# Kernel optimization log

Hardware: AMD Instinct MI355X
Metric: run time of the kernel (lower is better)

Reference implementation:

```python
import jax, jax.numpy as jnp
import numpy as np

N_NODES = 50000
N_EDGES = 800000
IN_F = 128
HID = 64
OUT_F = 64
H = 1  # num_heads


def _gat_layer(x, W, al, ar, b, src, dst, n_nodes):
    # DGL GATConv: project, per-head attention logits, edge softmax over dst, scatter-sum
    h, f = al.shape
    feat = (x @ W).reshape(x.shape[0], h, f)              # [N,H,F]
    el = jnp.sum(feat * al, axis=-1)                       # [N,H]
    er = jnp.sum(feat * ar, axis=-1)                       # [N,H]
    e = jax.nn.leaky_relu(el[src] + er[dst], negative_slope=0.2)  # [E,H]
    emax = jax.ops.segment_max(e, dst, num_segments=n_nodes)      # [N,H]
    ex = jnp.exp(e - emax[dst])                            # [E,H]
    denom = jax.ops.segment_sum(ex, dst, num_segments=n_nodes)    # [N,H]
    alpha = ex / denom[dst]                                # [E,H] edge softmax
    msg = feat[src] * alpha[:, :, None]                    # [E,H,F]
    out = jax.ops.segment_sum(msg, dst, num_segments=n_nodes) + b # [N,H,F]
    return out


def setup_inputs() -> dict:
    key = jax.random.key(0)
    ks = jax.random.split(key, 20)

    def glorot(k, shape, fan_in):
        return jax.random.normal(k, shape, dtype=jnp.float32) / np.sqrt(fan_in)

    x = jax.random.normal(ks[0], (N_NODES, IN_F), dtype=jnp.float32)
    src = jax.random.randint(ks[1], (N_EDGES,), 0, N_NODES, dtype=jnp.int32)
    dst = jax.random.randint(ks[2], (N_EDGES,), 0, N_NODES, dtype=jnp.int32)
    neg_src = jax.random.randint(ks[3], (N_EDGES,), 0, N_NODES, dtype=jnp.int32)
    neg_dst = jax.random.randint(ks[4], (N_EDGES,), 0, N_NODES, dtype=jnp.int32)

    # layer dims: 128 -> 64 -> 128 -> 64 (hidden, hidden*2, out), H=1, mean over heads
    W1 = glorot(ks[5], (IN_F, H * HID), IN_F)
    al1 = glorot(ks[6], (H, HID), HID)
    ar1 = glorot(ks[7], (H, HID), HID)
    b1 = jnp.zeros((H, HID), dtype=jnp.float32)
    W2 = glorot(ks[8], (HID, H * 2 * HID), HID)
    al2 = glorot(ks[9], (H, 2 * HID), 2 * HID)
    ar2 = glorot(ks[10], (H, 2 * HID), 2 * HID)
    b2 = jnp.zeros((H, 2 * HID), dtype=jnp.float32)
    W3 = glorot(ks[11], (2 * HID, H * OUT_F), 2 * HID)
    al3 = glorot(ks[12], (H, OUT_F), OUT_F)
    ar3 = glorot(ks[13], (H, OUT_F), OUT_F)
    b3 = jnp.zeros((H, OUT_F), dtype=jnp.float32)
    lp_W = glorot(ks[14], (2 * OUT_F, 1), 2 * OUT_F)
    lp_b = jnp.zeros((1,), dtype=jnp.float32)

    return {
        "x": x, "W1": W1, "al1": al1, "ar1": ar1, "b1": b1,
        "W2": W2, "al2": al2, "ar2": ar2, "b2": b2,
        "W3": W3, "al3": al3, "ar3": ar3, "b3": b3,
        "lp_W": lp_W, "lp_b": lp_b,
        "src": src, "dst": dst, "neg_src": neg_src, "neg_dst": neg_dst,
    }


def reference(x, W1, al1, ar1, b1, W2, al2, ar2, b2, W3, al3, ar3, b3,
              lp_W, lp_b, src, dst, neg_src, neg_dst):
    n = x.shape[0]
    h = jax.nn.relu(_gat_layer(x, W1, al1, ar1, b1, src, dst, n)).mean(axis=1)
    h = jax.nn.relu(_gat_layer(h, W2, al2, ar2, b2, src, dst, n)).mean(axis=1)
    h = _gat_layer(h, W3, al3, ar3, b3, src, dst, n).mean(axis=1)      # [N,OUT_F]
    pos_score = (jnp.concatenate([h[src], h[dst]], axis=1) @ lp_W + lp_b)[:, 0]
    neg_score = (jnp.concatenate([h[neg_src], h[neg_dst]], axis=1) @ lp_W + lp_b)[:, 0]
    return h, pos_score, neg_score
```

## Files before the change

### kernel.cpp

```cpp
#include <hip/hip_runtime.h>
#include <hip/hip_bf16.h>

#define NN 50000
#define NE 800000
#define NBKT 196
#define NT 200
#define TILE 4000

typedef unsigned short ushort_t;
typedef unsigned int uint_t;

typedef __bf16 bf16_t;
typedef bf16_t bf16x8 __attribute__((ext_vector_type(8)));
typedef float f32x4 __attribute__((ext_vector_type(4)));

__device__ __forceinline__ float leaky(float v) { return (v >= 0.f) ? v : 0.2f * v; }
__device__ __forceinline__ ushort_t f2bf(float f) {
    __hip_bfloat16 h = __float2bfloat16(f);
    return *reinterpret_cast<ushort_t*>(&h);
}
__device__ __forceinline__ float bf_lo(uint_t v) { return __uint_as_float(v << 16); }
__device__ __forceinline__ float bf_hi(uint_t v) { return __uint_as_float(v & 0xFFFF0000u); }


#define XBLK 3125
#define WELEM (128 * 64 * 3)
#define WBLK 96

__global__ void prep_hist(const float* __restrict__ X, ushort_t* __restrict__ Xbf,
                          const float* __restrict__ W1, const float* __restrict__ W2,
                          const float* __restrict__ W3, ushort_t* __restrict__ Wt1,
                          ushort_t* __restrict__ Wt2, ushort_t* __restrict__ Wt3,
                          const float* __restrict__ al2, const float* __restrict__ ar2,
                          float* __restrict__ val2, float* __restrict__ var2,
                          const int* __restrict__ dst, uint_t* __restrict__ gh) {
    __shared__ uint_t h[NBKT];
    int tid = threadIdx.x;
    int blk = blockIdx.x;
    if (blk < NT) {
        for (int i = tid; i < NBKT; i += 256) h[i] = 0;
        __syncthreads();
        int e0 = blk * TILE;
        for (int i = tid; i < TILE; i += 256)
            atomicAdd(&h[((uint_t)dst[e0 + i]) >> 8], 1u);
        __syncthreads();
        for (int i = tid; i < NBKT; i += 256) gh[(size_t)i * NT + blk] = h[i];
        return;
    }
    blk -= NT;
    if (blk < XBLK) {
        int i = blk * 256 + tid;
        const float4* p = reinterpret_cast<const float4*>(X + (size_t)i * 8);
        float4 a = p[0], b = p[1];
        uint4 o;
        o.x = ((uint_t)f2bf(a.y) << 16) | f2bf(a.x);
        o.y = ((uint_t)f2bf(a.w) << 16) | f2bf(a.z);
        o.z = ((uint_t)f2bf(b.y) << 16) | f2bf(b.x);
        o.w = ((uint_t)f2bf(b.w) << 16) | f2bf(b.z);
        *reinterpret_cast<uint4*>(Xbf + (size_t)i * 8) = o;
        return;
    }
    blk -= XBLK;
    if (blk < WBLK) {
        int gw = blk * 256 + tid;
        if (gw < 128 * 64) {
            int i = gw; int k = i >> 6, m = i & 63;
            Wt1[m * 128 + k] = f2bf(W1[i]);
        } else if (gw < 2 * 128 * 64) {
            int i = gw - 128 * 64; int k = i >> 7, m = i & 127;
            Wt2[m * 64 + k] = f2bf(W2[i]);
        } else if (gw < WELEM) {
            int i = gw - 2 * 128 * 64; int k = i >> 6, m = i & 63;
            Wt3[m * 128 + k] = f2bf(W3[i]);
        }
        return;
    }
    if (tid < 128) {
        int k = tid & 63;
        const float* av = (tid < 64) ? al2 : ar2;
        float acc = 0.f;
        const float* row = W2 + k * 128;
        #pragma unroll 8
        for (int m = 0; m < 128; ++m) acc += row[m] * av[m];
        if (tid < 64) val2[k] = acc; else var2[k] = acc;
    }
}


__global__ void scan_gh(uint_t* __restrict__ gh, uint_t* __restrict__ bucketbase) {
    int b = threadIdx.x;
    uint_t run = 0;
    if (b < NBKT) {
        uint_t* row = gh + (size_t)b * NT;
        #pragma unroll 8
        for (int t = 0; t < NT; ++t) { uint_t v = row[t]; row[t] = run; run += v; }
    }
    int lane = b & 63, w = b >> 6;
    uint_t sc = run;
    for (int o = 1; o < 64; o <<= 1) {
        uint_t x = __shfl_up(sc, o);
        if (lane >= o) sc += x;
    }
    __shared__ uint_t ws4[4];
    if (lane == 63) ws4[w] = sc;
    __syncthreads();
    if (b == 0) { uint_t r = 0; for (int i = 0; i < 4; ++i) { uint_t tmp = ws4[i]; ws4[i] = r; r += tmp; } }
    __syncthreads();
    uint_t excl = ws4[w] + sc - run;
    if (b < NBKT) {
        bucketbase[b] = excl;
        uint_t* row = gh + (size_t)b * NT;
        #pragma unroll 8
        for (int t = 0; t < NT; ++t) row[t] += excl;
    }
    if (b == NBKT - 1) bucketbase[NBKT] = excl + run;
}

__global__ void part_scatter(const int* __restrict__ src, const int* __restrict__ dst,
                             const uint_t* __restrict__ gh, uint_t* __restrict__ pairbuf) {
    __shared__ uint_t cur[NBKT];
    int t = blockIdx.x, tid = threadIdx.x;
    for (int i = tid; i < NBKT; i += 256) cur[i] = gh[(size_t)i * NT + t];
    __syncthreads();
    int e0 = t * TILE;
    for (int i = tid; i < TILE; i += 256) {
        int d = dst[e0 + i], s = src[e0 + i];
        uint_t pos = atomicAdd(&cur[((uint_t)d) >> 8], 1u);
        pairbuf[pos] = (uint_t)s | (((uint_t)d & 255u) << 16);
    }
}

__device__ __forceinline__ void gemm64_core(const ushort_t* __restrict__ Xbf,
                                            const ushort_t* __restrict__ Wt,
                                            const float* __restrict__ al,
                                            const float* __restrict__ ar,
                                            ushort_t* __restrict__ featbf,
                                            float* __restrict__ el, float* __restrict__ er,
                                            int N, int blk, int tid) {
    constexpr int CT = 4, KI = 4;
    int wv = tid >> 6, lane = tid & 63;
    int c = lane & 15, kq = lane >> 4;
    int n0 = blk * 64 + wv * 16;
    if (n0 >= N) return;

    const ushort_t* aptr = Xbf + (size_t)(n0 + c) * 128 + kq * 8;
    bf16x8 a[KI];
    #pragma unroll
    for (int ki = 0; ki < KI; ++ki)
        a[ki] = *reinterpret_cast<const bf16x8*>(aptr + ki * 32);

    f32x4 acc[CT];
    #pragma unroll
    for (int ct = 0; ct < CT; ++ct) acc[ct] = (f32x4){0.f, 0.f, 0.f, 0.f};

    #pragma unroll
    for (int ct = 0; ct < CT; ++ct) {
        const ushort_t* bptr = Wt + (size_t)(ct * 16 + c) * 128 + kq * 8;
        #pragma unroll
        for (int ki = 0; ki < KI; ++ki) {
            bf16x8 b = *reinterpret_cast<const bf16x8*>(bptr + ki * 32);
            acc[ct] = __builtin_amdgcn_mfma_f32_16x16x32_bf16(a[ki], b, acc[ct], 0, 0, 0);
        }
    }

    float pe[4] = {0.f, 0.f, 0.f, 0.f}, pr[4] = {0.f, 0.f, 0.f, 0.f};
    #pragma unroll
    for (int ct = 0; ct < CT; ++ct) {
        float alv = al[ct * 16 + c], arv = ar[ct * 16 + c];
        #pragma unroll
        for (int j = 0; j < 4; ++j) {
            float v = acc[ct][j];
            featbf[(size_t)(n0 + kq * 4 + j) * 64 + ct * 16 + c] = f2bf(v);
            pe[j] += v * alv;
            pr[j] += v * arv;
        }
    }
    #pragma unroll
    for (int o = 1; o < 16; o <<= 1) {
        #pragma unroll
        for (int j = 0; j < 4; ++j) {
            pe[j] += __shfl_xor(pe[j], o);
            pr[j] += __shfl_xor(pr[j], o);
        }
    }
    if (c == 0) {
        #pragma unroll
        for (int j = 0; j < 4; ++j) {
            el[n0 + kq * 4 + j] = pe[j];
            er[n0 + kq * 4 + j] = pr[j];
        }
    }
}

__global__ void csr_gemm1(const uint_t* __restrict__ pairbuf, const uint_t* __restrict__ bucketbase,
                          int* __restrict__ off, int* __restrict__ csrsrc,
                          const ushort_t* __restrict__ Xbf, const ushort_t* __restrict__ Wt1,
                          const float* __restrict__ al1, const float* __restrict__ ar1,
                          ushort_t* __restrict__ featbf, float* __restrict__ el,
                          float* __restrict__ er, int N) {
    __shared__ uint_t cnt[256];
    __shared__ uint_t ws4[4];
    int tid = threadIdx.x;
    if (blockIdx.x >= NBKT) {
        gemm64_core(Xbf, Wt1, al1, ar1, featbf, el, er, N, blockIdx.x - NBKT, tid);
        return;
    }
    int b = blockIdx.x;
    uint_t eb0 = bucketbase[b], m = bucketbase[b + 1] - eb0;
    cnt[tid] = 0;
    __syncthreads();
    for (uint_t i = tid; i < m; i += 256)
        atomicAdd(&cnt[pairbuf[eb0 + i] >> 16], 1u);
    __syncthreads();
    uint_t v = cnt[tid];
    int lane = tid & 63, w = tid >> 6;
    uint_t sc = v;
    for (int o = 1; o < 64; o <<= 1) {
        uint_t x = __shfl_up(sc, o);
        if (lane >= o) sc += x;
    }
    if (lane == 63) ws4[w] = sc;
    __syncthreads();
    if (tid == 0) { uint_t r = 0; for (int i = 0; i < 4; ++i) { uint_t tmp = ws4[i]; ws4[i] = r; r += tmp; } }
    __syncthreads();
    uint_t excl = ws4[w] + sc - v;
    int node = b * 256 + tid;
    if (node < NN) off[node] = (int)(eb0 + excl);
    if (b == 0 && tid == 0) off[NN] = NE;
    __syncthreads();
    cnt[tid] = eb0 + excl;
    __syncthreads();
    for (uint_t i = tid; i < m; i += 256) {
        uint_t p = pairbuf[eb0 + i];
        uint_t pos = atomicAdd(&cnt[p >> 16], 1u);
        csrsrc[pos] = (int)(p & 0xFFFFu);
    }
}

__global__ void fused_l23(const ushort_t* __restrict__ G, const ushort_t* __restrict__ Wt2,
                          const float* __restrict__ b2, const ushort_t* __restrict__ Wt3,
                          const float* __restrict__ al3, const float* __restrict__ ar3,
                          ushort_t* __restrict__ feat3, float* __restrict__ el,
                          float* __restrict__ er, int N) {
    __shared__ ushort_t h3s[4][16 * 128];
    int wv = threadIdx.x >> 6, lane = threadIdx.x & 63;
    int c = lane & 15, kq = lane >> 4;
    int n0 = blockIdx.x * 64 + wv * 16;
    if (n0 >= N) return;

    const ushort_t* aptr = G + (size_t)(n0 + c) * 64 + kq * 8;
    bf16x8 a1[2];
    a1[0] = *reinterpret_cast<const bf16x8*>(aptr);
    a1[1] = *reinterpret_cast<const bf16x8*>(aptr + 32);

    f32x4 acc2[8];
    #pragma unroll
    for (int ct = 0; ct < 8; ++ct) acc2[ct] = (f32x4){0.f, 0.f, 0.f, 0.f};
    #pragma unroll
    for (int ct = 0; ct < 8; ++ct) {
        const ushort_t* bptr = Wt2 + (size_t)(ct * 16 + c) * 64 + kq * 8;
        acc2[ct] = __builtin_amdgcn_mfma_f32_16x16x32_bf16(
            a1[0], *reinterpret_cast<const bf16x8*>(bptr), acc2[ct], 0, 0, 0);
        acc2[ct] = __builtin_amdgcn_mfma_f32_16x16x32_bf16(
            a1[1], *reinterpret_cast<const bf16x8*>(bptr + 32), acc2[ct], 0, 0, 0);
    }

    #pragma unroll
    for (int ct = 0; ct < 8; ++ct) {
        float bv = b2[ct * 16 + c];
        #pragma unroll
        for (int j = 0; j < 4; ++j) {
            int r = kq * 4 + j;
            float v = fmaxf(acc2[ct][j] + bv, 0.f);
            h3s[wv][r * 128 + ((ct * 16 + c) ^ ((r & 7) << 3))] = f2bf(v);
        }
    }

    bf16x8 a2[4];
    #pragma unroll
    for (int ki = 0; ki < 4; ++ki)
        a2[ki] = *reinterpret_cast<const bf16x8*>(
            &h3s[wv][c * 128 + ((ki * 32 + kq * 8) ^ ((c & 7) << 3))]);

    f32x4 acc3[4];
    #pragma unroll
    for (int ct = 0; ct < 4; ++ct) acc3[ct] = (f32x4){0.f, 0.f, 0.f, 0.f};
    #pragma unroll
    for (int ct = 0; ct < 4; ++ct) {
        const ushort_t* bptr = Wt3 + (size_t)(ct * 16 + c) * 128 + kq * 8;
        #pragma unroll
        for (int ki = 0; ki < 4; ++ki) {
            bf16x8 b = *reinterpret_cast<const bf16x8*>(bptr + ki * 32);
            acc3[ct] = __builtin_amdgcn_mfma_f32_16x16x32_bf16(a2[ki], b, acc3[ct], 0, 0, 0);
        }
    }

    float pe[4] = {0.f, 0.f, 0.f, 0.f}, pr[4] = {0.f, 0.f, 0.f, 0.f};
    #pragma unroll
    for (int ct = 0; ct < 4; ++ct) {
        float alv = al3[ct * 16 + c], arv = ar3[ct * 16 + c];
        #pragma unroll
        for (int j = 0; j < 4; ++j) {
            float v = acc3[ct][j];
            feat3[(size_t)(n0 + kq * 4 + j) * 64 + ct * 16 + c] = f2bf(v);
            pe[j] += v * alv;
            pr[j] += v * arv;
        }
    }
    #pragma unroll
    for (int o = 1; o < 16; o <<= 1) {
        #pragma unroll
        for (int j = 0; j < 4; ++j) {
            pe[j] += __shfl_xor(pe[j], o);
            pr[j] += __shfl_xor(pr[j], o);
        }
    }
    if (c == 0) {
        #pragma unroll
        for (int j = 0; j < 4; ++j) {
            el[n0 + kq * 4 + j] = pe[j];
            er[n0 + kq * 4 + j] = pr[j];
        }
    }
}

template <bool BIAS, bool RELU, bool BFOUT, bool DOTS>
__global__ void gat_agg2(const int* __restrict__ off, const int* __restrict__ csrsrc,
                         const float* __restrict__ el, const float* __restrict__ er,
                         const ushort_t* __restrict__ featbf, const float* __restrict__ bias,
                         void* __restrict__ hout, const float* __restrict__ va,
                         const float* __restrict__ vb, float* __restrict__ o1,
                         float* __restrict__ o2, int N) {
    int g = blockIdx.x * blockDim.x + threadIdx.x;
    int node = g >> 5;
    int sub = threadIdx.x & 31;
    if (node >= N) return;
    int start = off[node], deg = off[node + 1] - start;
    float ern = er[node];

    int s0 = 0; float e0 = -1e30f;
    if (sub < deg) { s0 = csrsrc[start + sub]; e0 = leaky(el[s0] + ern); }
    float m = e0;
    for (int i = 32 + sub; i < deg; i += 32)
        m = fmaxf(m, leaky(el[csrsrc[start + i]] + ern));
    for (int o = 16; o; o >>= 1) m = fmaxf(m, __shfl_xor(m, o));

    float p0 = (sub < deg) ? __expf(e0 - m) : 0.f;
    float ssum = p0;
    for (int i = 32 + sub; i < deg; i += 32)
        ssum += __expf(leaky(el[csrsrc[start + i]] + ern) - m);
    for (int o = 16; o; o >>= 1) ssum += __shfl_xor(ssum, o);
    float inv = (deg > 0) ? 1.f / ssum : 0.f;

    float acc0 = 0.f, acc1 = 0.f;
    int head = (deg < 32) ? deg : 32;
    int i = 0;
    for (; i + 4 <= head; i += 4) {
        float pA = __shfl(p0, i, 32), pB = __shfl(p0, i + 1, 32),
              pC = __shfl(p0, i + 2, 32), pD = __shfl(p0, i + 3, 32);
        int sA = __shfl(s0, i, 32), sB = __shfl(s0, i + 1, 32),
            sC = __shfl(s0, i + 2, 32), sD = __shfl(s0, i + 3, 32);
        uint_t vA = ((const uint_t*)(featbf + (size_t)sA * 64))[sub];
        uint_t vB = ((const uint_t*)(featbf + (size_t)sB * 64))[sub];
        uint_t vC = ((const uint_t*)(featbf + (size_t)sC * 64))[sub];
        uint_t vD = ((const uint_t*)(featbf + (size_t)sD * 64))[sub];
        acc0 += pA * bf_lo(vA) + pB * bf_lo(vB) + pC * bf_lo(vC) + pD * bf_lo(vD);
        acc1 += pA * bf_hi(vA) + pB * bf_hi(vB) + pC * bf_hi(vC) + pD * bf_hi(vD);
    }
    for (; i < head; ++i) {
        float p = __shfl(p0, i, 32);
        int sN = __shfl(s0, i, 32);
        uint_t v = ((const uint_t*)(featbf + (size_t)sN * 64))[sub];
        acc0 += p * bf_lo(v); acc1 += p * bf_hi(v);
    }
    for (i = 32; i < deg; ++i) {
        int sN = csrsrc[start + i];
        float p = __expf(leaky(el[sN] + ern) - m);
        uint_t v = ((const uint_t*)(featbf + (size_t)sN * 64))[sub];
        acc0 += p * bf_lo(v); acc1 += p * bf_hi(v);
    }

    float v0 = acc0 * inv, v1 = acc1 * inv;
    if (BIAS) {
        float2 b2 = ((const float2*)bias)[sub];
        v0 += b2.x; v1 += b2.y;
    }
    if (RELU) { v0 = fmaxf(v0, 0.f); v1 = fmaxf(v1, 0.f); }
    if (BFOUT) {
        ((uint_t*)hout)[(size_t)node * 32 + sub] = ((uint_t)f2bf(v1) << 16) | f2bf(v0);
    } else {
        ((float2*)hout)[(size_t)node * 32 + sub] = make_float2(v0, v1);
    }
    if (DOTS) {
        float2 wa = ((const float2*)va)[sub];
        float2 wb = ((const float2*)vb)[sub];
        float a = v0 * wa.x + v1 * wa.y;
        float b = v0 * wb.x + v1 * wb.y;
        for (int o = 16; o; o >>= 1) { a += __shfl_xor(a, o); b += __shfl_xor(b, o); }
        if (sub == 0) { o1[node] = a; o2[node] = b; }
    }
}

__global__ void scores4_k(const int4* __restrict__ s4, const int4* __restrict__ d4,
                          const int4* __restrict__ ns4, const int4* __restrict__ nd4,
                          const float* __restrict__ s1, const float* __restrict__ s2,
                          const float* __restrict__ lpb,
                          float4* __restrict__ outp, float4* __restrict__ outn, int E4) {
    int i = blockIdx.x * blockDim.x + threadIdx.x;
    float cc = lpb[0];
    if (i < E4) {
        int4 s = s4[i], d = d4[i];
        outp[i] = make_float4(s1[s.x] + s2[d.x] + cc, s1[s.y] + s2[d.y] + cc,
                              s1[s.z] + s2[d.z] + cc, s1[s.w] + s2[d.w] + cc);
    } else if (i < 2 * E4) {
        int j = i - E4;
        int4 s = ns4[j], d = nd4[j];
        outn[j] = make_float4(s1[s.x] + s2[d.x] + cc, s1[s.y] + s2[d.y] + cc,
                              s1[s.z] + s2[d.z] + cc, s1[s.w] + s2[d.w] + cc);
    }
}


struct Scratch {
    ushort_t* xbf; ushort_t* wt1; ushort_t* wt2; ushort_t* wt3;
    ushort_t* featbf; ushort_t* hAbf;
    float* elA; float* erA; float* elB; float* erB;
    float* val2; float* var2; float* s1; float* s2;
    int* off; int* csrsrc; uint_t* gh; uint_t* bucketbase;
    uint_t* pairbuf;
};

extern "C" void kernel_launch(void* const* d_in, const int* in_sizes, int n_in,
                              void* d_out, int out_size, void* d_ws, size_t ws_size,
                              hipStream_t stream) {
    const float* x   = (const float*)d_in[0];
    const float* W1  = (const float*)d_in[1];
    const float* al1 = (const float*)d_in[2];
    const float* ar1 = (const float*)d_in[3];
    const float* b1  = (const float*)d_in[4];
    const float* W2  = (const float*)d_in[5];
    const float* al2 = (const float*)d_in[6];
    const float* ar2 = (const float*)d_in[7];
    const float* b2  = (const float*)d_in[8];
    const float* W3  = (const float*)d_in[9];
    const float* al3 = (const float*)d_in[10];
    const float* ar3 = (const float*)d_in[11];
    const float* b3  = (const float*)d_in[12];
    const float* lpW = (const float*)d_in[13];
    const float* lpb = (const float*)d_in[14];
    const int* src  = (const int*)d_in[15];
    const int* dst  = (const int*)d_in[16];
    const int* nsrc = (const int*)d_in[17];
    const int* ndst = (const int*)d_in[18];

    char* w = (char*)d_ws;
    Scratch S;
    S.xbf        = (ushort_t*)w; w += (size_t)NN * 128 * 2;
    S.featbf     = (ushort_t*)w; w += (size_t)NN * 64 * 2;
    S.hAbf       = (ushort_t*)w; w += (size_t)NN * 64 * 2;
    S.wt1        = (ushort_t*)w; w += 128 * 64 * 2;
    S.wt2        = (ushort_t*)w; w += 64 * 128 * 2;
    S.wt3        = (ushort_t*)w; w += 128 * 64 * 2;
    S.elA        = (float*)w;    w += (size_t)NN * 4;
    S.erA        = (float*)w;    w += (size_t)NN * 4;
    S.elB        = (float*)w;    w += (size_t)NN * 4;
    S.erB        = (float*)w;    w += (size_t)NN * 4;
    S.val2       = (float*)w;    w += 64 * 4;
    S.var2       = (float*)w;    w += 64 * 4;
    S.s1         = (float*)w;    w += (size_t)NN * 4;
    S.s2         = (float*)w;    w += (size_t)NN * 4;
    S.off        = (int*)w;      w += (size_t)(NN + 1) * 4;
    S.csrsrc     = (int*)w;      w += (size_t)NE * 4;
    S.gh         = (uint_t*)w;   w += (size_t)NBKT * NT * 4;
    S.bucketbase = (uint_t*)w;   w += (size_t)(NBKT + 1) * 4;
    S.pairbuf    = (uint_t*)w;   w += (size_t)NE * 4;

    const int GEMM_GRID = (NN + 63) / 64;
    const int AGG_GRID = (NN * 32 + 255) / 256;

    prep_hist<<<NT + XBLK + WBLK + 1, 256, 0, stream>>>(
        x, S.xbf, W1, W2, W3, S.wt1, S.wt2, S.wt3, al2, ar2, S.val2, S.var2, dst, S.gh);
    scan_gh<<<1, 256, 0, stream>>>(S.gh, S.bucketbase);
    part_scatter<<<NT, 256, 0, stream>>>(src, dst, S.gh, S.pairbuf);
    csr_gemm1<<<NBKT + GEMM_GRID, 256, 0, stream>>>(
        S.pairbuf, S.bucketbase, S.off, S.csrsrc,
        S.xbf, S.wt1, al1, ar1, S.featbf, S.elA, S.erA, NN);

    float* out_h   = (float*)d_out;
    float* out_pos = out_h + (size_t)NN * 64;
    float* out_neg = out_pos + NE;

    gat_agg2<true, true, true, true><<<AGG_GRID, 256, 0, stream>>>(
        S.off, S.csrsrc, S.elA, S.erA, S.featbf, b1, S.hAbf,
        S.val2, S.var2, S.elB, S.erB, NN);
    gat_agg2<false, false, true, false><<<AGG_GRID, 256, 0, stream>>>(
        S.off, S.csrsrc, S.elB, S.erB, S.hAbf, nullptr, S.featbf,
        nullptr, nullptr, nullptr, nullptr, NN);
    fused_l23<<<GEMM_GRID, 256, 0, stream>>>(S.featbf, S.wt2, b2, S.wt3, al3, ar3,
                                             S.hAbf, S.elA, S.erA, NN);
    gat_agg2<true, false, false, true><<<AGG_GRID, 256, 0, stream>>>(
        S.off, S.csrsrc, S.elA, S.erA, S.hAbf, b3, out_h,
        lpW, lpW + 64, S.s1, S.s2, NN);
    const int E4 = NE / 4;
    scores4_k<<<(2 * E4 + 255) / 256, 256, 0, stream>>>(
        (const int4*)src, (const int4*)dst, (const int4*)nsrc, (const int4*)ndst,
        S.s1, S.s2, lpb, (float4*)out_pos, (float4*)out_neg, E4);
}
```

Before: 179.5 us.

## Fuse fp32-to-bf16 conversion of X into GEMM load and parallelize bucket scan

Drops the separate pass that converts X to bf16 in scratch memory. The layer-1 GEMM now loads fp32 rows directly and converts them in registers, which removes one write and one read of a 12.8MB-equivalent buffer. The single-block bucket-histogram scan now uses 1024 threads, with one wavefront scanning each bucket row through shuffles instead of a serial per-thread loop. The bucket base offset is no longer stored into every row of the histogram. part_scatter adds it when it initializes its cursors instead. The GEMM reads twice as many bytes for X, and each lane uses more load instructions.

```diff
diff --git a/kernel.cpp b/kernel.cpp
--- a/kernel.cpp
+++ b/kernel.cpp
@@ -23,12 +23,10 @@
 __device__ __forceinline__ float bf_hi(uint_t v) { return __uint_as_float(v & 0xFFFF0000u); }
 
 
-#define XBLK 3125
 #define WELEM (128 * 64 * 3)
 #define WBLK 96
 
-__global__ void prep_hist(const float* __restrict__ X, ushort_t* __restrict__ Xbf,
-                          const float* __restrict__ W1, const float* __restrict__ W2,
+__global__ void prep_hist(const float* __restrict__ W1, const float* __restrict__ W2,
                           const float* __restrict__ W3, ushort_t* __restrict__ Wt1,
                           ushort_t* __restrict__ Wt2, ushort_t* __restrict__ Wt3,
                           const float* __restrict__ al2, const float* __restrict__ ar2,
@@ -48,19 +46,6 @@
         return;
     }
     blk -= NT;
-    if (blk < XBLK) {
-        int i = blk * 256 + tid;
-        const float4* p = reinterpret_cast<const float4*>(X + (size_t)i * 8);
-        float4 a = p[0], b = p[1];
-        uint4 o;
-        o.x = ((uint_t)f2bf(a.y) << 16) | f2bf(a.x);
-        o.y = ((uint_t)f2bf(a.w) << 16) | f2bf(a.z);
-        o.z = ((uint_t)f2bf(b.y) << 16) | f2bf(b.x);
-        o.w = ((uint_t)f2bf(b.w) << 16) | f2bf(b.z);
-        *reinterpret_cast<uint4*>(Xbf + (size_t)i * 8) = o;
-        return;
-    }
-    blk -= XBLK;
     if (blk < WBLK) {
         int gw = blk * 256 + tid;
         if (gw < 128 * 64) {
@@ -86,41 +71,55 @@
     }
 }
 
-
 __global__ void scan_gh(uint_t* __restrict__ gh, uint_t* __restrict__ bucketbase) {
-    int b = threadIdx.x;
-    uint_t run = 0;
-    if (b < NBKT) {
+    __shared__ uint_t btot[NBKT];
+    __shared__ uint_t ws4[4];
+    int tid = threadIdx.x;
+    int wv = tid >> 6, lane = tid & 63;
+    for (int b = wv; b < NBKT; b += 16) {
         uint_t* row = gh + (size_t)b * NT;
-        #pragma unroll 8
-        for (int t = 0; t < NT; ++t) { uint_t v = row[t]; row[t] = run; run += v; }
-    }
-    int lane = b & 63, w = b >> 6;
-    uint_t sc = run;
-    for (int o = 1; o < 64; o <<= 1) {
-        uint_t x = __shfl_up(sc, o);
-        if (lane >= o) sc += x;
-    }
-    __shared__ uint_t ws4[4];
-    if (lane == 63) ws4[w] = sc;
-    __syncthreads();
-    if (b == 0) { uint_t r = 0; for (int i = 0; i < 4; ++i) { uint_t tmp = ws4[i]; ws4[i] = r; r += tmp; } }
-    __syncthreads();
-    uint_t excl = ws4[w] + sc - run;
-    if (b < NBKT) {
-        bucketbase[b] = excl;
-        uint_t* row = gh + (size_t)b * NT;
-        #pragma unroll 8
-        for (int t = 0; t < NT; ++t) row[t] += excl;
-    }
-    if (b == NBKT - 1) bucketbase[NBKT] = excl + run;
+        uint_t carry = 0;
+        for (int base = 0; base < NT; base += 64) {
+            int idx = base + lane;
+            uint_t v = (idx < NT) ? row[idx] : 0;
+            uint_t sc = v;
+            for (int o = 1; o < 64; o <<= 1) {
+                uint_t xx = __shfl_up(sc, o);
+                if (lane >= o) sc += xx;
+            }
+            if (idx < NT) row[idx] = carry + sc - v;
+            carry += __shfl(sc, 63);
+        }
+        if (lane == 0) btot[b] = carry;
+    }
+    __syncthreads();
+    uint_t v = 0, sc = 0;
+    if (tid < 256) {
+        v = (tid < NBKT) ? btot[tid] : 0;
+        sc = v;
+        for (int o = 1; o < 64; o <<= 1) {
+            uint_t xx = __shfl_up(sc, o);
+            if ((tid & 63) >= o) sc += xx;
+        }
+        if ((tid & 63) == 63) ws4[tid >> 6] = sc;
+    }
+    __syncthreads();
+    if (tid == 0) {
+        uint_t r = 0;
+        for (int i = 0; i < 4; ++i) { uint_t tmp = ws4[i]; ws4[i] = r; r += tmp; }
+    }
+    __syncthreads();
+    if (tid < NBKT) bucketbase[tid] = ws4[tid >> 6] + sc - v;
+    if (tid == 0) bucketbase[NBKT] = NE;
 }
 
 __global__ void part_scatter(const int* __restrict__ src, const int* __restrict__ dst,
-                             const uint_t* __restrict__ gh, uint_t* __restrict__ pairbuf) {
+                             const uint_t* __restrict__ gh, const uint_t* __restrict__ bucketbase,
+                             uint_t* __restrict__ pairbuf) {
     __shared__ uint_t cur[NBKT];
     int t = blockIdx.x, tid = threadIdx.x;
-    for (int i = tid; i < NBKT; i += 256) cur[i] = gh[(size_t)i * NT + t];
+    for (int i = tid; i < NBKT; i += 256)
+        cur[i] = gh[(size_t)i * NT + t] + bucketbase[i];
     __syncthreads();
     int e0 = t * TILE;
     for (int i = tid; i < TILE; i += 256) {
@@ -130,24 +129,30 @@
     }
 }
 
-__device__ __forceinline__ void gemm64_core(const ushort_t* __restrict__ Xbf,
-                                            const ushort_t* __restrict__ Wt,
-                                            const float* __restrict__ al,
-                                            const float* __restrict__ ar,
-                                            ushort_t* __restrict__ featbf,
-                                            float* __restrict__ el, float* __restrict__ er,
-                                            int N, int blk, int tid) {
+__device__ __forceinline__ void gemm64_f32core(const float* __restrict__ X,
+                                               const ushort_t* __restrict__ Wt,
+                                               const float* __restrict__ al,
+                                               const float* __restrict__ ar,
+                                               ushort_t* __restrict__ featbf,
+                                               float* __restrict__ el, float* __restrict__ er,
+                                               int N, int blk, int tid) {
     constexpr int CT = 4, KI = 4;
     int wv = tid >> 6, lane = tid & 63;
     int c = lane & 15, kq = lane >> 4;
     int n0 = blk * 64 + wv * 16;
     if (n0 >= N) return;
 
-    const ushort_t* aptr = Xbf + (size_t)(n0 + c) * 128 + kq * 8;
+    const float* aptr = X + (size_t)(n0 + c) * 128 + kq * 8;
     bf16x8 a[KI];
     #pragma unroll
-    for (int ki = 0; ki < KI; ++ki)
-        a[ki] = *reinterpret_cast<const bf16x8*>(aptr + ki * 32);
+    for (int ki = 0; ki < KI; ++ki) {
+        float4 f0 = *reinterpret_cast<const float4*>(aptr + ki * 32);
+        float4 f1 = *reinterpret_cast<const float4*>(aptr + ki * 32 + 4);
+        union { bf16x8 v; ushort_t u[8]; } pk;
+        pk.u[0] = f2bf(f0.x); pk.u[1] = f2bf(f0.y); pk.u[2] = f2bf(f0.z); pk.u[3] = f2bf(f0.w);
+        pk.u[4] = f2bf(f1.x); pk.u[5] = f2bf(f1.y); pk.u[6] = f2bf(f1.z); pk.u[7] = f2bf(f1.w);
+        a[ki] = pk.v;
+    }
 
     f32x4 acc[CT];
     #pragma unroll
@@ -194,7 +199,7 @@
 
 __global__ void csr_gemm1(const uint_t* __restrict__ pairbuf, const uint_t* __restrict__ bucketbase,
                           int* __restrict__ off, int* __restrict__ csrsrc,
-                          const ushort_t* __restrict__ Xbf, const ushort_t* __restrict__ Wt1,
+                          const float* __restrict__ X, const ushort_t* __restrict__ Wt1,
                           const float* __restrict__ al1, const float* __restrict__ ar1,
                           ushort_t* __restrict__ featbf, float* __restrict__ el,
                           float* __restrict__ er, int N) {
@@ -202,7 +207,7 @@
     __shared__ uint_t ws4[4];
     int tid = threadIdx.x;
     if (blockIdx.x >= NBKT) {
-        gemm64_core(Xbf, Wt1, al1, ar1, featbf, el, er, N, blockIdx.x - NBKT, tid);
+        gemm64_f32core(X, Wt1, al1, ar1, featbf, el, er, N, blockIdx.x - NBKT, tid);
         return;
     }
     int b = blockIdx.x;
@@ -422,7 +427,7 @@
 
 
 struct Scratch {
-    ushort_t* xbf; ushort_t* wt1; ushort_t* wt2; ushort_t* wt3;
+    ushort_t* wt1; ushort_t* wt2; ushort_t* wt3;
     ushort_t* featbf; ushort_t* hAbf;
     float* elA; float* erA; float* elB; float* erB;
     float* val2; float* var2; float* s1; float* s2;
@@ -455,7 +460,6 @@
 
     char* w = (char*)d_ws;
     Scratch S;
-    S.xbf        = (ushort_t*)w; w += (size_t)NN * 128 * 2;
     S.featbf     = (ushort_t*)w; w += (size_t)NN * 64 * 2;
     S.hAbf       = (ushort_t*)w; w += (size_t)NN * 64 * 2;
     S.wt1        = (ushort_t*)w; w += 128 * 64 * 2;
@@ -478,13 +482,13 @@
     const int GEMM_GRID = (NN + 63) / 64;
     const int AGG_GRID = (NN * 32 + 255) / 256;
 
-    prep_hist<<<NT + XBLK + WBLK + 1, 256, 0, stream>>>(
-        x, S.xbf, W1, W2, W3, S.wt1, S.wt2, S.wt3, al2, ar2, S.val2, S.var2, dst, S.gh);
-    scan_gh<<<1, 256, 0, stream>>>(S.gh, S.bucketbase);
-    part_scatter<<<NT, 256, 0, stream>>>(src, dst, S.gh, S.pairbuf);
+    prep_hist<<<NT + WBLK + 1, 256, 0, stream>>>(
+        W1, W2, W3, S.wt1, S.wt2, S.wt3, al2, ar2, S.val2, S.var2, dst, S.gh);
+    scan_gh<<<1, 1024, 0, stream>>>(S.gh, S.bucketbase);
+    part_scatter<<<NT, 256, 0, stream>>>(src, dst, S.gh, S.bucketbase, S.pairbuf);
     csr_gemm1<<<NBKT + GEMM_GRID, 256, 0, stream>>>(
         S.pairbuf, S.bucketbase, S.off, S.csrsrc,
-        S.xbf, S.wt1, al1, ar1, S.featbf, S.elA, S.erA, NN);
+        x, S.wt1, al1, ar1, S.featbf, S.elA, S.erA, NN);
 
     float* out_h   = (float*)d_out;
     float* out_pos = out_h + (size_t)NN * 64;
```

Measured after the change: 164.0 us. 8.7% less time.
